# Kernel optimization log

Hardware: AMD Instinct MI355X
Metric: run time of the kernel (lower is better)

The kernel has to match this reference:

```python
import jax, jax.numpy as jnp
import numpy as np

D_MODEL = 2048
NUM_HEADS = 16
HEAD_DIM = D_MODEL // NUM_HEADS
D_FF = 8192
EPS = 1e-6


def rmsnorm(x, w):
    return x * jax.lax.rsqrt(jnp.mean(x * x, axis=-1, keepdims=True) + EPS) * w


def setup_inputs() -> dict:
    key = jax.random.key(0)
    ks = jax.random.split(key, 8)
    B, S, D = 2, 2048, D_MODEL
    s = lambda d: 1.0 / np.sqrt(d)
    return {
        "x": jax.random.normal(ks[0], (B, S, D), dtype=jnp.float32),
        "w_qkv": jax.random.normal(ks[1], (D, 3 * D), dtype=jnp.float32) * s(D),
        "w_out": jax.random.normal(ks[2], (D, D), dtype=jnp.float32) * s(D),
        "w1": jax.random.normal(ks[3], (D, D_FF), dtype=jnp.float32) * s(D),
        "w2": jax.random.normal(ks[4], (D_FF, D), dtype=jnp.float32) * s(D_FF),
        "w3": jax.random.normal(ks[5], (D, D_FF), dtype=jnp.float32) * s(D),
        "g1": jnp.ones((D,), dtype=jnp.float32),
        "g2": jnp.ones((D,), dtype=jnp.float32),
    }


def attention(x, w_qkv, w_out):
    B, S, D = x.shape
    H, Hd = NUM_HEADS, HEAD_DIM
    qkv = (x @ w_qkv).reshape(B, S, 3, H, Hd)
    q = qkv[:, :, 0].transpose(0, 2, 1, 3)  # [B,H,S,Hd]
    k = qkv[:, :, 1].transpose(0, 2, 1, 3)
    v = qkv[:, :, 2].transpose(0, 2, 1, 3)
    scale = Hd ** -0.5
    attn = jnp.einsum("bhqd,bhkd->bhqk", q, k) * scale
    causal = jnp.tril(jnp.ones((S, S), dtype=bool))
    attn = jnp.where(causal, attn, -jnp.inf)
    attn = jax.nn.softmax(attn, axis=-1)
    out = jnp.einsum("bhqk,bhkd->bhqd", attn, v)
    out = out.transpose(0, 2, 1, 3).reshape(B, S, D)
    return out @ w_out


def ffn(x, w1, w2, w3):
    return (jax.nn.silu(x @ w1) * (x @ w3)) @ w2


def reference(x, w_qkv, w_out, w1, w2, w3, g1, g2):
    x = x + attention(rmsnorm(x, g1), w_qkv, w_out)
    return x + ffn(rmsnorm(x, g2), w1, w2, w3)
```

## Files before the change

kernel.cpp:

```cpp
#include <hip/hip_runtime.h>
#include <cstdint>
#include <cstddef>

typedef __bf16 bf16x8 __attribute__((ext_vector_type(8)));
typedef float f32x4 __attribute__((ext_vector_type(4)));

__device__ __forceinline__ void gl_lds16(const void* g, void* l) {
  __builtin_amdgcn_global_load_lds(
      (const __attribute__((address_space(1))) void*)g,
      (__attribute__((address_space(3))) void*)l, 16, 0, 0);
}

__global__ __launch_bounds__(256) void wconv_t_k(const float* __restrict__ W,
                                                 __bf16* __restrict__ WT,
                                                 int K, int N) {
  __shared__ float tile[32][33];
  const int c0 = blockIdx.x * 32, r0 = blockIdx.y * 32;
  const int tx = threadIdx.x & 31, ty = threadIdx.x >> 5;
#pragma unroll
  for (int i = 0; i < 32; i += 8)
    tile[ty + i][tx] = W[(size_t)(r0 + ty + i) * N + c0 + tx];
  __syncthreads();
#pragma unroll
  for (int i = 0; i < 32; i += 8)
    WT[(size_t)(c0 + ty + i) * K + r0 + tx] = (__bf16)tile[tx][ty + i];
}

__global__ __launch_bounds__(256) void rmsnorm_k(const float* __restrict__ x,
                                                 const float* __restrict__ g,
                                                 __bf16* __restrict__ out) {
  constexpr int D = 2048;
  const int row = blockIdx.x, t = threadIdx.x;
  const float4* xr = (const float4*)(x + (size_t)row * D);
  float4 a = xr[t * 2], b2 = xr[t * 2 + 1];
  float ss = a.x * a.x + a.y * a.y + a.z * a.z + a.w * a.w +
             b2.x * b2.x + b2.y * b2.y + b2.z * b2.z + b2.w * b2.w;
#pragma unroll
  for (int d = 1; d < 64; d <<= 1) ss += __shfl_xor(ss, d, 64);
  __shared__ float red[4];
  if ((t & 63) == 0) red[t >> 6] = ss;
  __syncthreads();
  float rs = rsqrtf((red[0] + red[1] + red[2] + red[3]) * (1.f / D) + 1e-6f);
  const float4* gr = (const float4*)g;
  float4 ga = gr[t * 2], gb = gr[t * 2 + 1];
  bf16x8 o8;
  o8[0] = (__bf16)(a.x * rs * ga.x);
  o8[1] = (__bf16)(a.y * rs * ga.y);
  o8[2] = (__bf16)(a.z * rs * ga.z);
  o8[3] = (__bf16)(a.w * rs * ga.w);
  o8[4] = (__bf16)(b2.x * rs * gb.x);
  o8[5] = (__bf16)(b2.y * rs * gb.y);
  o8[6] = (__bf16)(b2.z * rs * gb.z);
  o8[7] = (__bf16)(b2.w * rs * gb.w);
  *(bf16x8*)(out + (size_t)row * D + t * 8) = o8;
}

__global__ __launch_bounds__(256) void addrms_k(const float* __restrict__ p0,
                                                const float* __restrict__ p1,
                                                const float* __restrict__ res,
                                                const float* __restrict__ g,
                                                float* __restrict__ hout,
                                                __bf16* __restrict__ xnout) {
  constexpr int D = 2048;
  const int row = blockIdx.x, t = threadIdx.x;
  const size_t base = (size_t)row * D;
  float4 h[2];
#pragma unroll
  for (int j = 0; j < 2; ++j) {
    float4 a = ((const float4*)(p0 + base))[t * 2 + j];
    float4 b = ((const float4*)(p1 + base))[t * 2 + j];
    float4 c = ((const float4*)(res + base))[t * 2 + j];
    h[j].x = a.x + b.x + c.x; h[j].y = a.y + b.y + c.y;
    h[j].z = a.z + b.z + c.z; h[j].w = a.w + b.w + c.w;
    ((float4*)(hout + base))[t * 2 + j] = h[j];
  }
  float ss = h[0].x * h[0].x + h[0].y * h[0].y + h[0].z * h[0].z + h[0].w * h[0].w +
             h[1].x * h[1].x + h[1].y * h[1].y + h[1].z * h[1].z + h[1].w * h[1].w;
#pragma unroll
  for (int d = 1; d < 64; d <<= 1) ss += __shfl_xor(ss, d, 64);
  __shared__ float red[4];
  if ((t & 63) == 0) red[t >> 6] = ss;
  __syncthreads();
  float rs = rsqrtf((red[0] + red[1] + red[2] + red[3]) * (1.f / D) + 1e-6f);
  const float4* gr = (const float4*)g;
  float4 ga = gr[t * 2], gb = gr[t * 2 + 1];
  bf16x8 o8;
  o8[0] = (__bf16)(h[0].x * rs * ga.x);
  o8[1] = (__bf16)(h[0].y * rs * ga.y);
  o8[2] = (__bf16)(h[0].z * rs * ga.z);
  o8[3] = (__bf16)(h[0].w * rs * ga.w);
  o8[4] = (__bf16)(h[1].x * rs * gb.x);
  o8[5] = (__bf16)(h[1].y * rs * gb.y);
  o8[6] = (__bf16)(h[1].z * rs * gb.z);
  o8[7] = (__bf16)(h[1].w * rs * gb.w);
  *(bf16x8*)(xnout + base + t * 8) = o8;
}

__global__ __launch_bounds__(256) void addred_k(const float* __restrict__ p0,
                                                const float* __restrict__ p1,
                                                const float* __restrict__ res,
                                                float* __restrict__ out, int n4) {
  int i = blockIdx.x * 256 + threadIdx.x;
  const int stride = gridDim.x * 256;
  for (; i < n4; i += stride) {
    float4 a = ((const float4*)p0)[i];
    float4 b = ((const float4*)p1)[i];
    float4 c = ((const float4*)res)[i];
    float4 o = {a.x + b.x + c.x, a.y + b.y + c.y, a.z + b.z + c.z, a.w + b.w + c.w};
    ((float4*)out)[i] = o;
  }
}

#define RD_A(BUF, HALF) do {                                        \
  const __bf16* aT_ = &As[BUF][0] + aoff + (HALF) * 4096;           \
  _Pragma("unroll")                                                 \
  for (int mi = 0; mi < 4; ++mi) {                                  \
    Ar[mi][0] = *(const bf16x8*)(aT_ + mi * 1024 + k0off);          \
    Ar[mi][1] = *(const bf16x8*)(aT_ + mi * 1024 + k1off);          \
  } } while (0)

#define RD_B(BUF, NH) do {                                          \
  const __bf16* bT_ = &Bs[BUF][0] + boff + (NH) * 2048;             \
  _Pragma("unroll")                                                 \
  for (int ni = 0; ni < 2; ++ni) {                                  \
    Br[NH][ni][0] = *(const bf16x8*)(bT_ + ni * 1024 + k0off);      \
    Br[NH][ni][1] = *(const bf16x8*)(bT_ + ni * 1024 + k1off);      \
  } } while (0)

#define MQ(MH, NH) do {                                             \
  __builtin_amdgcn_s_setprio(1);                                    \
  _Pragma("unroll")                                                 \
  for (int mi = 0; mi < 4; ++mi) {                                  \
    _Pragma("unroll")                                               \
    for (int ni = 0; ni < 2; ++ni) {                                \
      f32x4& a_ = acc[(MH) * 4 + mi][(NH) * 2 + ni];                \
      a_ = __builtin_amdgcn_mfma_f32_16x16x32_bf16(Ar[mi][0], Br[NH][ni][0], a_, 0, 0, 0); \
      a_ = __builtin_amdgcn_mfma_f32_16x16x32_bf16(Ar[mi][1], Br[NH][ni][1], a_, 0, 0, 0); \
    } }                                                             \
  __builtin_amdgcn_s_setprio(0);                                    \
} while (0)

#define PEND(VM) do {                                               \
  __builtin_amdgcn_sched_barrier(0);                                \
  asm volatile("s_waitcnt vmcnt(" #VM ")" ::: "memory");            \
  __builtin_amdgcn_s_barrier();                                     \
  __builtin_amdgcn_sched_barrier(0);                                \
} while (0)

#define PEND_NOVM() do {                                            \
  __builtin_amdgcn_sched_barrier(0);                                \
  __builtin_amdgcn_s_barrier();                                     \
  __builtin_amdgcn_sched_barrier(0);                                \
} while (0)

#define KTILE(BUF, STG0, STG1, STG2, STG3, END0, END1, END2, END3) do { \
  RD_A(BUF, 0); RD_B(BUF, 0); RD_B(BUF, 1);                         \
  MQ(0, 0); STG0; END0;                                             \
  MQ(0, 1); RD_A(BUF, 1); STG1; END1;                               \
  MQ(1, 1); STG2; END2;                                             \
  MQ(1, 0); STG3; END3;                                             \
} while (0)

template <int MODE>
__global__ __launch_bounds__(512, 2) void gemm8_k(
    const __bf16* __restrict__ A, const __bf16* __restrict__ BT,
    const float* __restrict__ res, const __bf16* __restrict__ aux,
    void* __restrict__ Cout, int M, int N, int K, int lda, int cswz) {
  __shared__ alignas(16) __bf16 As[2][256 * 64];
  __shared__ alignas(16) __bf16 Bs[2][256 * 64];
  const int tid = threadIdx.x;
  const int lane = tid & 63, w = tid >> 6;
  const int wm = w >> 2, wn = w & 3;
  const int l15 = lane & 15, l16 = lane >> 4;

  const int nbx = gridDim.x, nby = gridDim.y;
  const int nwg = nbx * nby;
  const int bid = blockIdx.y * nbx + blockIdx.x;
  const int swz = (bid & 7) * (nwg >> 3) + (bid >> 3);
  int bx, by;
  if (cswz) { by = swz % nby; bx = swz / nby; }
  else      { bx = swz % nbx; by = swz / nbx; }
  const int m0 = by * 256, n0 = bx * 256;
  const int nkt = K >> 6;

  float* CoutF = (float*)Cout;
  if constexpr (MODE == 4) {
    const int z = blockIdx.z;
    A += (size_t)z * K;
    BT += (size_t)z * K;
    CoutF += (size_t)z * M * N;
  }

  const int srow = tid >> 3;
  const int scole = ((tid & 7) * 8) ^ ((srow & 7) << 3);
  const int brow_i = ((tid >> 8) << 6) + ((tid >> 3) & 31);

  auto stgA = [&](int t, int h) {
    if (t < nkt) {
      char* dst = (char*)(&As[t & 1][0]) + h * 8192 + tid * 16;
      const __bf16* src = A + (size_t)(m0 + h * 64 + srow) * lda + t * 64 + scole;
      gl_lds16(src, dst);
      gl_lds16(src + (size_t)128 * lda, dst + 16384);
    }
  };
  auto stgB = [&](int t, int h) {
    if (t < nkt) {
      const int r = h * 32 + brow_i;
      char* dst = (char*)(&Bs[t & 1][0]) + r * 128 + (tid & 7) * 16;
      const __bf16* src = BT + (size_t)(n0 + r) * lda + t * 64 + scole;
      gl_lds16(src, dst);
      gl_lds16(src + (size_t)128 * lda, dst + 16384);
    }
  };

  const int rswz = (l15 & 7) << 3;
  const int k0off = (l16 * 8) ^ rswz;
  const int k1off = (32 + l16 * 8) ^ rswz;
  const int aoff = (wm * 128 + l15) * 64;
  const int boff = (wn * 64 + l15) * 64;

  f32x4 acc[8][4] = {};
  bf16x8 Ar[4][2], Br[2][2][2];

  stgA(0, 0); stgB(0, 0); stgB(0, 1); stgA(0, 1);
  stgA(1, 0); stgB(1, 0);
  asm volatile("s_waitcnt vmcnt(6)" ::: "memory");
  __builtin_amdgcn_s_barrier();
  __builtin_amdgcn_sched_barrier(0);

  int t = 0;
  for (; t + 3 < nkt; t += 2) {
    KTILE(0, stgB(t + 1, 1), stgA(t + 1, 1), stgA(t + 2, 0), stgB(t + 2, 0),
          PEND(6), PEND_NOVM(), PEND_NOVM(), PEND(6));
    KTILE(1, stgB(t + 2, 1), stgA(t + 2, 1), stgA(t + 3, 0), stgB(t + 3, 0),
          PEND(6), PEND_NOVM(), PEND_NOVM(), PEND(6));
  }
  KTILE(0, stgB(t + 1, 1), stgA(t + 1, 1), (void)0, (void)0,
        PEND(6), PEND_NOVM(), PEND_NOVM(), PEND(2));
  KTILE(1, (void)0, (void)0, (void)0, (void)0,
        PEND(0), PEND_NOVM(), PEND_NOVM(), (void)0);

#pragma unroll
  for (int m = 0; m < 8; ++m) {
    const int rowb = m0 + wm * 128 + m * 16 + l16 * 4;
#pragma unroll
    for (int n = 0; n < 4; ++n) {
      const int col = n0 + wn * 64 + n * 16 + l15;
#pragma unroll
      for (int r = 0; r < 4; ++r) {
        const size_t idx = (size_t)(rowb + r) * N + col;
        float v = acc[m][n][r];
        if constexpr (MODE == 1) {
          CoutF[idx] = v + res[idx];
        } else if constexpr (MODE == 2) {
          float s = v / (1.f + __expf(-v));
          ((__bf16*)Cout)[idx] = (__bf16)s;
        } else if constexpr (MODE == 3) {
          ((__bf16*)Cout)[idx] = (__bf16)(v * (float)aux[idx]);
        } else if constexpr (MODE == 4) {
          CoutF[idx] = v;
        } else {
          ((__bf16*)Cout)[idx] = (__bf16)v;
        }
      }
    }
  }
}

__global__ __launch_bounds__(256) void vtrans_k(const __bf16* __restrict__ qkv,
                                                __bf16* __restrict__ VT) {
  constexpr int S = 2048;
  __shared__ __bf16 tile[64][65];
  const int s0 = blockIdx.x * 64, d0 = blockIdx.y * 64;
  const int bh = blockIdx.z, b = bh >> 4, h = bh & 15;
  const int tx = threadIdx.x & 63, ty = threadIdx.x >> 6;
  const size_t vbase = ((size_t)b * S * 3 + 2) * 2048 + h * 128;
#pragma unroll
  for (int i = 0; i < 16; ++i) {
    int s = ty + i * 4;
    tile[s][tx] = qkv[vbase + (size_t)(s0 + s) * 6144 + d0 + tx];
  }
  __syncthreads();
  const size_t obase = ((size_t)bh * 128 + d0) * S + s0;
#pragma unroll
  for (int i = 0; i < 16; ++i) {
    int d = ty + i * 4;
    VT[obase + (size_t)d * S + tx] = tile[tx][d];
  }
}

__global__ __launch_bounds__(512) void attn_k(const __bf16* __restrict__ qkv,
                                              const __bf16* __restrict__ VT,
                                              __bf16* __restrict__ out) {
  constexpr int S = 2048;
  const int bid = blockIdx.x;
  const int bh = (bid & 7) * 4 + ((bid >> 3) & 3);
  const int qb = 15 - (bid >> 5);
  const int b = bh >> 4, h = bh & 15;
  const int q0 = qb * 128;
  const int tid = threadIdx.x, lane = tid & 63, w = tid >> 6;
  const int l15 = lane & 15, l16 = lane >> 4;

  __shared__ __bf16 Ks[64 * 128];
  __shared__ __bf16 Vs[128 * 64];
  __shared__ __bf16 Ps[8][16 * 72];

  const size_t qbase = (size_t)b * S * 6144 + h * 128;
  const size_t kbase = qbase + 2048;
  const size_t vtbase = (size_t)bh * 128 * 2048;

  bf16x8 qf[4];
  {
    const __bf16* qp = qkv + qbase + (size_t)(q0 + w * 16 + l15) * 6144 + l16 * 8;
#pragma unroll
    for (int kc = 0; kc < 4; ++kc) qf[kc] = *(const bf16x8*)(qp + kc * 32);
  }

  f32x4 o[8] = {};
  float mrow[4] = {-1e30f, -1e30f, -1e30f, -1e30f};
  float lrow[4] = {0.f, 0.f, 0.f, 0.f};
  const float sm = 0.08838834764831845f * 1.4426950408889634f;

  int ksrow[2], kscol[2], vsrow[2], vscol[2];
#pragma unroll
  for (int c = 0; c < 2; ++c) {
    int P = (c * 512 + tid) * 16;
    int kr = P >> 8;
    ksrow[c] = kr;
    kscol[c] = ((P & 255) ^ ((kr & 7) << 4)) >> 1;
    int vr = P >> 7;
    vsrow[c] = vr;
    vscol[c] = ((P & 127) ^ ((vr & 7) << 4)) >> 1;
  }
  const int fswz = (l15 & 7) << 3;
  const int qrow_abs = q0 + w * 16 + l16 * 4;

#pragma unroll
  for (int c = 0; c < 2; ++c) {
    int e = (c * 512 + tid) * 8;
    gl_lds16(qkv + kbase + (size_t)ksrow[c] * 6144 + kscol[c], &Ks[e]);
    gl_lds16(VT + vtbase + (size_t)vsrow[c] * 2048 + vscol[c], &Vs[e]);
  }

  const int ntk = 2 * qb + 2;
  for (int kt = 0; kt < ntk; ++kt) {
    const int k0 = kt * 64;
    __syncthreads();

    bf16x8 kreg[2], vreg[2];
    const bool pf = kt + 1 < ntk;
    if (pf) {
      const int kn = k0 + 64;
#pragma unroll
      for (int c = 0; c < 2; ++c)
        kreg[c] = *(const bf16x8*)(qkv + kbase + (size_t)(kn + ksrow[c]) * 6144 + kscol[c]);
#pragma unroll
      for (int c = 0; c < 2; ++c)
        vreg[c] = *(const bf16x8*)(VT + vtbase + (size_t)vsrow[c] * 2048 + kn + vscol[c]);
    }

    f32x4 s4[4];
    __builtin_amdgcn_s_setprio(1);
#pragma unroll
    for (int f = 0; f < 4; ++f) {
      f32x4 accs = {};
#pragma unroll
      for (int kc = 0; kc < 4; ++kc) {
        bf16x8 kf = *(const bf16x8*)&Ks[(f * 16 + l15) * 128 + ((kc * 32 + l16 * 8) ^ fswz)];
        accs = __builtin_amdgcn_mfma_f32_16x16x32_bf16(qf[kc], kf, accs, 0, 0, 0);
      }
      s4[f] = accs;
    }
    __builtin_amdgcn_s_setprio(0);

    float pm[4] = {-1e30f, -1e30f, -1e30f, -1e30f};
    float pvv[4][4];
#pragma unroll
    for (int f = 0; f < 4; ++f) {
      const int key = k0 + f * 16 + l15;
#pragma unroll
      for (int r = 0; r < 4; ++r) {
        float s = s4[f][r] * sm;
        if (key > qrow_abs + r) s = -1e30f;
        pvv[f][r] = s;
        pm[r] = fmaxf(pm[r], s);
      }
    }
#pragma unroll
    for (int d = 1; d < 16; d <<= 1) {
#pragma unroll
      for (int r = 0; r < 4; ++r) pm[r] = fmaxf(pm[r], __shfl_xor(pm[r], d, 64));
    }
    float fac[4], ts[4];
#pragma unroll
    for (int r = 0; r < 4; ++r) {
      float mn = fmaxf(mrow[r], pm[r]);
      fac[r] = exp2f(mrow[r] - mn);
      mrow[r] = mn;
      ts[r] = 0.f;
    }
#pragma unroll
    for (int f = 0; f < 4; ++f) {
#pragma unroll
      for (int r = 0; r < 4; ++r) {
        float p = exp2f(pvv[f][r] - mrow[r]);
        ts[r] += p;
        Ps[w][(l16 * 4 + r) * 72 + f * 16 + l15] = (__bf16)p;
      }
    }
#pragma unroll
    for (int d = 1; d < 16; d <<= 1) {
#pragma unroll
      for (int r = 0; r < 4; ++r) ts[r] += __shfl_xor(ts[r], d, 64);
    }
#pragma unroll
    for (int r = 0; r < 4; ++r) lrow[r] = lrow[r] * fac[r] + ts[r];
#pragma unroll
    for (int n = 0; n < 8; ++n) {
      o[n][0] *= fac[0];
      o[n][1] *= fac[1];
      o[n][2] *= fac[2];
      o[n][3] *= fac[3];
    }
    __builtin_amdgcn_s_setprio(1);
#pragma unroll
    for (int kc = 0; kc < 2; ++kc) {
      bf16x8 pf2 = *(const bf16x8*)&Ps[w][l15 * 72 + kc * 32 + l16 * 8];
#pragma unroll
      for (int n = 0; n < 8; ++n) {
        bf16x8 vf = *(const bf16x8*)&Vs[(n * 16 + l15) * 64 + ((kc * 32 + l16 * 8) ^ fswz)];
        o[n] = __builtin_amdgcn_mfma_f32_16x16x32_bf16(pf2, vf, o[n], 0, 0, 0);
      }
    }
    __builtin_amdgcn_s_setprio(0);
    __syncthreads();

    if (pf) {
#pragma unroll
      for (int c = 0; c < 2; ++c) *(bf16x8*)&Ks[(c * 512 + tid) * 8] = kreg[c];
#pragma unroll
      for (int c = 0; c < 2; ++c) *(bf16x8*)&Vs[(c * 512 + tid) * 8] = vreg[c];
    }
  }

  const int orow = b * S + q0 + w * 16 + l16 * 4;
#pragma unroll
  for (int r = 0; r < 4; ++r) {
    const float inv = 1.f / lrow[r];
#pragma unroll
    for (int n = 0; n < 8; ++n)
      out[(size_t)(orow + r) * 2048 + h * 128 + n * 16 + l15] = (__bf16)(o[n][r] * inv);
  }
}

extern "C" void kernel_launch(void* const* d_in, const int* in_sizes, int n_in,
                              void* d_out, int out_size, void* d_ws, size_t ws_size,
                              hipStream_t stream) {
  (void)in_sizes; (void)n_in; (void)out_size; (void)ws_size;
  const float* x = (const float*)d_in[0];
  const float* w_qkv = (const float*)d_in[1];
  const float* w_out = (const float*)d_in[2];
  const float* w1 = (const float*)d_in[3];
  const float* w2 = (const float*)d_in[4];
  const float* w3 = (const float*)d_in[5];
  const float* g1 = (const float*)d_in[6];
  const float* g2 = (const float*)d_in[7];
  char* ws = (char*)d_ws;

  constexpr int Mr = 4096, D = 2048, DFF = 8192, TD = 6144;

  __bf16* wqkvT = (__bf16*)(ws + 0);
  __bf16* w1T   = (__bf16*)(ws + 0);
  __bf16* woutT = (__bf16*)(ws + 33554432);
  __bf16* qkvb  = (__bf16*)(ws + 41943040);
  __bf16* w3T   = (__bf16*)(ws + 41943040);
  __bf16* w2T   = (__bf16*)(ws + 75497472);
  __bf16* VTb   = (__bf16*)(ws + 92274688);
  __bf16* xn    = (__bf16*)(ws + 109051904);
  __bf16* attn  = (__bf16*)(ws + 125829120);
  float*  hbuf  = (float*)(ws + 142606336);
  __bf16* gbuf  = (__bf16*)(ws + 176160768);
  float*  pO    = (float*)(ws + 176160768);
  float*  pW0   = (float*)(ws + 0);

  wconv_t_k<<<dim3(TD / 32, D / 32), 256, 0, stream>>>(w_qkv, wqkvT, D, TD);
  wconv_t_k<<<dim3(D / 32, D / 32), 256, 0, stream>>>(w_out, woutT, D, D);
  rmsnorm_k<<<Mr, 256, 0, stream>>>(x, g1, xn);
  gemm8_k<0><<<dim3(TD / 256, Mr / 256), 512, 0, stream>>>(xn, wqkvT, nullptr, nullptr, qkvb, Mr, TD, D, D, 1);
  vtrans_k<<<dim3(32, 2, 32), 256, 0, stream>>>(qkvb, VTb);
  attn_k<<<512, 512, 0, stream>>>(qkvb, VTb, attn);
  gemm8_k<4><<<dim3(D / 256, Mr / 256, 2), 512, 0, stream>>>(attn, woutT, nullptr, nullptr, pO, Mr, D, D / 2, D, 0);
  addrms_k<<<Mr, 256, 0, stream>>>(pO, pO + (size_t)Mr * D, x, g2, hbuf, xn);
  wconv_t_k<<<dim3(DFF / 32, D / 32), 256, 0, stream>>>(w1, w1T, D, DFF);
  wconv_t_k<<<dim3(DFF / 32, D / 32), 256, 0, stream>>>(w3, w3T, D, DFF);
  wconv_t_k<<<dim3(D / 32, DFF / 32), 256, 0, stream>>>(w2, w2T, DFF, D);
  gemm8_k<2><<<dim3(DFF / 256, Mr / 256), 512, 0, stream>>>(xn, w1T, nullptr, nullptr, gbuf, Mr, DFF, D, D, 1);
  gemm8_k<3><<<dim3(DFF / 256, Mr / 256), 512, 0, stream>>>(xn, w3T, nullptr, gbuf, gbuf, Mr, DFF, D, D, 1);
  gemm8_k<4><<<dim3(D / 256, Mr / 256, 2), 512, 0, stream>>>(gbuf, w2T, nullptr, nullptr, pW0, Mr, D, DFF / 2, DFF, 0);
  addred_k<<<2048, 256, 0, stream>>>(pW0, pW0 + (size_t)Mr * D, hbuf, (float*)d_out, Mr * D / 4);
}
```

Measured before the change: 737.0 us.

## Fuse final residual add into split-K W2 GEMM via atomics; widen weight transpose tiles

The addrms kernel now also writes the residual sum straight into the output buffer. The split-K W2 GEMM then atomically adds its partial results into that buffer, which removes the separate reduction kernel and the fp32 partial-buffer round trip. The weight transpose kernel moves to 64x64 tiles with float4 loads and 4-wide bf16 stores to improve memory coalescing. The atomics add contention and make the summation order nondeterministic. They also run scalar per element, which may cost more than the removed kernel.

```diff
diff --git a/kernel.cpp b/kernel.cpp
--- a/kernel.cpp
+++ b/kernel.cpp
@@ -3,6 +3,7 @@
 #include <cstddef>
 
 typedef __bf16 bf16x8 __attribute__((ext_vector_type(8)));
+typedef __bf16 bf16x4 __attribute__((ext_vector_type(4)));
 typedef float f32x4 __attribute__((ext_vector_type(4)));
 
 __device__ __forceinline__ void gl_lds16(const void* g, void* l) {
@@ -14,16 +15,28 @@
 __global__ __launch_bounds__(256) void wconv_t_k(const float* __restrict__ W,
                                                  __bf16* __restrict__ WT,
                                                  int K, int N) {
-  __shared__ float tile[32][33];
-  const int c0 = blockIdx.x * 32, r0 = blockIdx.y * 32;
-  const int tx = threadIdx.x & 31, ty = threadIdx.x >> 5;
-#pragma unroll
-  for (int i = 0; i < 32; i += 8)
-    tile[ty + i][tx] = W[(size_t)(r0 + ty + i) * N + c0 + tx];
+  __shared__ float tile[64][68];
+  const int c0 = blockIdx.x * 64, r0 = blockIdx.y * 64;
+  const int t = threadIdx.x;
+  const int lr = t >> 4;
+  const int lc = (t & 15) * 4;
+#pragma unroll
+  for (int i = 0; i < 4; ++i) {
+    float4 v = *(const float4*)&W[(size_t)(r0 + lr + i * 16) * N + c0 + lc];
+    *(float4*)&tile[lr + i * 16][lc] = v;
+  }
   __syncthreads();
-#pragma unroll
-  for (int i = 0; i < 32; i += 8)
-    WT[(size_t)(c0 + ty + i) * K + r0 + tx] = (__bf16)tile[tx][ty + i];
+  const int cr = t >> 4, kb = (t & 15) * 4;
+#pragma unroll
+  for (int j = 0; j < 4; ++j) {
+    const int c = cr + j * 16;
+    bf16x4 o;
+    o[0] = (__bf16)tile[kb + 0][c];
+    o[1] = (__bf16)tile[kb + 1][c];
+    o[2] = (__bf16)tile[kb + 2][c];
+    o[3] = (__bf16)tile[kb + 3][c];
+    *(bf16x4*)&WT[(size_t)(c0 + c) * K + r0 + kb] = o;
+  }
 }
 
 __global__ __launch_bounds__(256) void rmsnorm_k(const float* __restrict__ x,
@@ -60,7 +73,8 @@
                                                 const float* __restrict__ res,
                                                 const float* __restrict__ g,
                                                 float* __restrict__ hout,
-                                                __bf16* __restrict__ xnout) {
+                                                __bf16* __restrict__ xnout,
+                                                float* __restrict__ dres) {
   constexpr int D = 2048;
   const int row = blockIdx.x, t = threadIdx.x;
   const size_t base = (size_t)row * D;
@@ -73,6 +87,7 @@
     h[j].x = a.x + b.x + c.x; h[j].y = a.y + b.y + c.y;
     h[j].z = a.z + b.z + c.z; h[j].w = a.w + b.w + c.w;
     ((float4*)(hout + base))[t * 2 + j] = h[j];
+    ((float4*)(dres + base))[t * 2 + j] = h[j];
   }
   float ss = h[0].x * h[0].x + h[0].y * h[0].y + h[0].z * h[0].z + h[0].w * h[0].w +
              h[1].x * h[1].x + h[1].y * h[1].y + h[1].z * h[1].z + h[1].w * h[1].w;
@@ -96,21 +111,6 @@
   *(bf16x8*)(xnout + base + t * 8) = o8;
 }
 
-__global__ __launch_bounds__(256) void addred_k(const float* __restrict__ p0,
-                                                const float* __restrict__ p1,
-                                                const float* __restrict__ res,
-                                                float* __restrict__ out, int n4) {
-  int i = blockIdx.x * 256 + threadIdx.x;
-  const int stride = gridDim.x * 256;
-  for (; i < n4; i += stride) {
-    float4 a = ((const float4*)p0)[i];
-    float4 b = ((const float4*)p1)[i];
-    float4 c = ((const float4*)res)[i];
-    float4 o = {a.x + b.x + c.x, a.y + b.y + c.y, a.z + b.z + c.z, a.w + b.w + c.w};
-    ((float4*)out)[i] = o;
-  }
-}
-
 #define RD_A(BUF, HALF) do {                                        \
   const __bf16* aT_ = &As[BUF][0] + aoff + (HALF) * 4096;           \
   _Pragma("unroll")                                                 \
@@ -184,11 +184,11 @@
   const int nkt = K >> 6;
 
   float* CoutF = (float*)Cout;
-  if constexpr (MODE == 4) {
+  if constexpr (MODE == 4 || MODE == 5) {
     const int z = blockIdx.z;
     A += (size_t)z * K;
     BT += (size_t)z * K;
-    CoutF += (size_t)z * M * N;
+    if constexpr (MODE == 4) CoutF += (size_t)z * M * N;
   }
 
   const int srow = tid >> 3;
@@ -259,6 +259,8 @@
           ((__bf16*)Cout)[idx] = (__bf16)(v * (float)aux[idx]);
         } else if constexpr (MODE == 4) {
           CoutF[idx] = v;
+        } else if constexpr (MODE == 5) {
+          atomicAdd(&CoutF[idx], v);
         } else {
           ((__bf16*)Cout)[idx] = (__bf16)v;
         }
@@ -481,21 +483,19 @@
   float*  hbuf  = (float*)(ws + 142606336);
   __bf16* gbuf  = (__bf16*)(ws + 176160768);
   float*  pO    = (float*)(ws + 176160768);
-  float*  pW0   = (float*)(ws + 0);
-
-  wconv_t_k<<<dim3(TD / 32, D / 32), 256, 0, stream>>>(w_qkv, wqkvT, D, TD);
-  wconv_t_k<<<dim3(D / 32, D / 32), 256, 0, stream>>>(w_out, woutT, D, D);
+
+  wconv_t_k<<<dim3(TD / 64, D / 64), 256, 0, stream>>>(w_qkv, wqkvT, D, TD);
+  wconv_t_k<<<dim3(D / 64, D / 64), 256, 0, stream>>>(w_out, woutT, D, D);
   rmsnorm_k<<<Mr, 256, 0, stream>>>(x, g1, xn);
   gemm8_k<0><<<dim3(TD / 256, Mr / 256), 512, 0, stream>>>(xn, wqkvT, nullptr, nullptr, qkvb, Mr, TD, D, D, 1);
   vtrans_k<<<dim3(32, 2, 32), 256, 0, stream>>>(qkvb, VTb);
   attn_k<<<512, 512, 0, stream>>>(qkvb, VTb, attn);
   gemm8_k<4><<<dim3(D / 256, Mr / 256, 2), 512, 0, stream>>>(attn, woutT, nullptr, nullptr, pO, Mr, D, D / 2, D, 0);
-  addrms_k<<<Mr, 256, 0, stream>>>(pO, pO + (size_t)Mr * D, x, g2, hbuf, xn);
-  wconv_t_k<<<dim3(DFF / 32, D / 32), 256, 0, stream>>>(w1, w1T, D, DFF);
-  wconv_t_k<<<dim3(DFF / 32, D / 32), 256, 0, stream>>>(w3, w3T, D, DFF);
-  wconv_t_k<<<dim3(D / 32, DFF / 32), 256, 0, stream>>>(w2, w2T, DFF, D);
+  addrms_k<<<Mr, 256, 0, stream>>>(pO, pO + (size_t)Mr * D, x, g2, hbuf, xn, (float*)d_out);
+  wconv_t_k<<<dim3(DFF / 64, D / 64), 256, 0, stream>>>(w1, w1T, D, DFF);
+  wconv_t_k<<<dim3(DFF / 64, D / 64), 256, 0, stream>>>(w3, w3T, D, DFF);
+  wconv_t_k<<<dim3(D / 64, DFF / 64), 256, 0, stream>>>(w2, w2T, DFF, D);
   gemm8_k<2><<<dim3(DFF / 256, Mr / 256), 512, 0, stream>>>(xn, w1T, nullptr, nullptr, gbuf, Mr, DFF, D, D, 1);
   gemm8_k<3><<<dim3(DFF / 256, Mr / 256), 512, 0, stream>>>(xn, w3T, nullptr, gbuf, gbuf, Mr, DFF, D, D, 1);
-  gemm8_k<4><<<dim3(D / 256, Mr / 256, 2), 512, 0, stream>>>(gbuf, w2T, nullptr, nullptr, pW0, Mr, D, DFF / 2, DFF, 0);
-  addred_k<<<2048, 256, 0, stream>>>(pW0, pW0 + (size_t)Mr * D, hbuf, (float*)d_out, Mr * D / 4);
-}
+  gemm8_k<5><<<dim3(D / 256, Mr / 256, 2), 512, 0, stream>>>(gbuf, w2T, nullptr, nullptr, (float*)d_out, Mr, D, DFF / 2, DFF, 0);
+}
```

Measured after the change: 756.5 us. 2.6% more time.
